# Kernel tuning notes

Measured on AMD Instinct MI355X. Metric: run time of the kernel, lower is better.

## Reference

```python
import jax, jax.numpy as jnp
import numpy as np

N = 100000
E = 1600000
D_IN = 128
D_H = 128
D_OUT = 128
LN_EPS = 1e-5
NORM_EPS = 1e-12


def _sage_conv(x, src, dst, Wl, bl, Wr):
    # PyG SAGEConv(mean): out = lin_l(mean_{j in N(i)} x_j) + lin_r(x_i)
    msgs = x[src]                                             # [E, d] gather
    summed = jax.ops.segment_sum(msgs, dst, num_segments=N)   # [N, d]
    cnt = jax.ops.segment_sum(jnp.ones((src.shape[0],), x.dtype), dst, num_segments=N)
    mean = summed / jnp.maximum(cnt, 1.0)[:, None]
    return mean @ Wl + bl + x @ Wr


def _layer_norm(x, g, b):
    mu = jnp.mean(x, axis=-1, keepdims=True)
    var = jnp.mean(jnp.square(x - mu), axis=-1, keepdims=True)
    return (x - mu) * jax.lax.rsqrt(var + LN_EPS) * g + b


def setup_inputs() -> dict:
    key = jax.random.key(0)
    ks = jax.random.split(key, 20)
    x = jax.random.normal(ks[0], (N, D_IN), dtype=jnp.float32)
    edge_index = jax.random.randint(ks[1], (2, E), 0, N, dtype=jnp.int64)
    dims = [(D_IN, D_H), (D_H, D_H), (D_H, D_OUT)]
    inp = {"x": x, "edge_index": edge_index}
    for i, (di, do) in enumerate(dims):
        s = 1.0 / np.sqrt(di)
        inp[f"Wl{i}"] = jax.random.normal(ks[2 + 5 * i], (di, do), dtype=jnp.float32) * s
        inp[f"bl{i}"] = jnp.zeros((do,), dtype=jnp.float32)
        inp[f"Wr{i}"] = jax.random.normal(ks[3 + 5 * i], (di, do), dtype=jnp.float32) * s
        inp[f"g{i}"] = jnp.ones((do,), dtype=jnp.float32)
        inp[f"b{i}"] = jnp.zeros((do,), dtype=jnp.float32)
    return inp


def reference(x, edge_index, Wl0, bl0, Wr0, g0, b0, Wl1, bl1, Wr1, g1, b1, Wl2, bl2, Wr2, g2, b2):
    src, dst = edge_index[0], edge_index[1]
    params = [(Wl0, bl0, Wr0, g0, b0), (Wl1, bl1, Wr1, g1, b1), (Wl2, bl2, Wr2, g2, b2)]
    h = x
    for i, (Wl, bl, Wr, g, b) in enumerate(params):
        h = _sage_conv(h, src, dst, Wl, bl, Wr)
        h = _layer_norm(h, g, b)
        if i < len(params) - 1:
            h = jax.nn.elu(h)
            # dropout is identity in eval mode
    # F.normalize(p=2, dim=-1)
    nrm = jnp.sqrt(jnp.sum(jnp.square(h), axis=-1, keepdims=True))
    return h / jnp.maximum(nrm, NORM_EPS)
```

## Files before the change

### kernel.cpp

```cpp
#include <hip/hip_runtime.h>
#include <hip/hip_bf16.h>
#include <math.h>

#define N_NODES 100000
#define N_EDGES 1600000
#define D 128
#define NB 391
#define BSTRIDE 6000

#define OFF_SSRC 0
#define OFF_OFFS 6400000
#define OFF_PACK 6800016
#define OFF_GC   7193232
#define OFF_BB   7195296
#define OFF_M    7204112
#define OFF_XHI  58404112
#define OFF_XLO  84004112

#define LSTRIDE 130

typedef __attribute__((ext_vector_type(8))) short short8;
typedef __attribute__((ext_vector_type(4))) float floatx4;

__device__ __forceinline__ unsigned short f2bf(float f) {
    unsigned int u = __float_as_uint(f);
    u += 0x7fffu + ((u >> 16) & 1u);
    return (unsigned short)(u >> 16);
}
__device__ __forceinline__ float bf2f(unsigned short h) {
    return __uint_as_float(((unsigned int)h) << 16);
}

__global__ __launch_bounds__(256) void part_kernel(const int* __restrict__ src,
                                                   const int* __restrict__ dst,
                                                   int* __restrict__ gcur,
                                                   uint2* __restrict__ staging) {
    __shared__ int hist[NB];
    __shared__ int base[NB];
    int t = threadIdx.x;
    int e0 = blockIdx.x * 4096;
    for (int i = t; i < NB; i += 256) hist[i] = 0;
    __syncthreads();
    int d[16];
#pragma unroll
    for (int i = 0; i < 16; ++i) {
        int e = e0 + i * 256 + t;
        d[i] = (e < N_EDGES) ? dst[e] : -1;
        if (d[i] >= 0) atomicAdd(&hist[d[i] >> 8], 1);
    }
    __syncthreads();
    for (int i = t; i < NB; i += 256) {
        int h = hist[i];
        base[i] = h ? atomicAdd(&gcur[i], h) : 0;
    }
    __syncthreads();
    for (int i = t; i < NB; i += 256) hist[i] = 0;
    __syncthreads();
#pragma unroll
    for (int i = 0; i < 16; ++i) {
        if (d[i] >= 0) {
            int e = e0 + i * 256 + t;
            int b = d[i] >> 8;
            int slot = atomicAdd(&hist[b], 1);
            staging[b * BSTRIDE + base[b] + slot] =
                make_uint2((unsigned)src[e], (unsigned)(d[i] & 255));
        }
    }
}

__global__ void bscan_kernel(const int* __restrict__ gcur, int* __restrict__ bbase,
                             int* __restrict__ offs) {
    __shared__ int sh[512];
    int t = threadIdx.x;
    int v = (t < NB) ? gcur[t] : 0;
    sh[t] = v;
    __syncthreads();
    for (int off = 1; off < 512; off <<= 1) {
        int y = (t >= off) ? sh[t - off] : 0;
        __syncthreads();
        sh[t] += y;
        __syncthreads();
    }
    if (t < NB) bbase[t] = sh[t] - v;
    if (t == 0) offs[N_NODES] = N_EDGES;
}

__global__ __launch_bounds__(256) void bsort_kernel(const uint2* __restrict__ staging,
                                                    const int* __restrict__ gcur,
                                                    const int* __restrict__ bbase,
                                                    int* __restrict__ offs,
                                                    int* __restrict__ s_src) {
    __shared__ int cnt[256];
    __shared__ int scn[256];
    __shared__ int ssrc[BSTRIDE];
    int b = blockIdx.x;
    int t = threadIdx.x;
    int n = gcur[b];
    int base_out = bbase[b];
    cnt[t] = 0;
    __syncthreads();
    for (int e = t; e < n; e += 256) {
        uint2 v = staging[b * BSTRIDE + e];
        atomicAdd(&cnt[v.y], 1);
    }
    __syncthreads();
    int v = cnt[t];
    scn[t] = v;
    __syncthreads();
    for (int off = 1; off < 256; off <<= 1) {
        int y = (t >= off) ? scn[t - off] : 0;
        __syncthreads();
        scn[t] += y;
        __syncthreads();
    }
    int ex = scn[t] - v;
    int node = b * 256 + t;
    if (node < N_NODES) offs[node] = base_out + ex;
    cnt[t] = ex;
    __syncthreads();
    for (int e = t; e < n; e += 256) {
        uint2 w = staging[b * BSTRIDE + e];
        int slot = atomicAdd(&cnt[w.y], 1);
        ssrc[slot] = (int)w.x;
    }
    __syncthreads();
    for (int e = t; e < n; e += 256) s_src[base_out + e] = ssrc[e];
}

__global__ void pack_kernel(const float* __restrict__ Wl0, const float* __restrict__ Wr0,
                            const float* __restrict__ Wl1, const float* __restrict__ Wr1,
                            const float* __restrict__ Wl2, const float* __restrict__ Wr2,
                            unsigned short* __restrict__ pack) {
    int tid = blockIdx.x * blockDim.x + threadIdx.x;
    int l = tid >> 15;
    int r = tid & 32767;
    int k = r >> 7;
    int n = r & 127;
    const float* Wl = (l == 0) ? Wl0 : (l == 1) ? Wl1 : Wl2;
    const float* Wr = (l == 0) ? Wr0 : (l == 1) ? Wr1 : Wr2;
    float v = (k < 128) ? Wl[k * 128 + n] : Wr[(k - 128) * 128 + n];
    unsigned short hi = f2bf(v);
    unsigned short lo = f2bf(v - bf2f(hi));
    int ct = n >> 4, ks = k >> 5, lane = ((k >> 3) & 3) * 16 + (n & 15), j = k & 7;
    int idx = ((ct * 8 + ks) * 64 + lane) * 8 + j;
    pack[l * 65536 + idx] = hi;
    pack[l * 65536 + 32768 + idx] = lo;
}

__global__ __launch_bounds__(256) void cvt_kernel(const float* __restrict__ x,
                                                  unsigned int* __restrict__ Xhi,
                                                  unsigned int* __restrict__ Xlo) {
    int i = blockIdx.x * 256 + threadIdx.x;
    float2 v = ((const float2*)x)[i];
    unsigned short h0 = f2bf(v.x), h1 = f2bf(v.y);
    unsigned short l0 = f2bf(v.x - bf2f(h0)), l1 = f2bf(v.y - bf2f(h1));
    Xhi[i] = (unsigned int)h0 | ((unsigned int)h1 << 16);
    Xlo[i] = (unsigned int)l0 | ((unsigned int)l1 << 16);
}

__global__ __launch_bounds__(128) void fused_kernel(const uint4* __restrict__ X4,
                                                    const unsigned short* __restrict__ Xh,
                                                    const unsigned short* __restrict__ Xl,
                                                    unsigned short* __restrict__ XhO,
                                                    unsigned short* __restrict__ XlO,
                                                    const int* __restrict__ s_src,
                                                    const int* __restrict__ offs,
                                                    const unsigned short* __restrict__ packh,
                                                    const unsigned short* __restrict__ packl,
                                                    const float* __restrict__ bl,
                                                    const float* __restrict__ g,
                                                    const float* __restrict__ b,
                                                    float* __restrict__ outf, int last) {
    __shared__ float lmean[64 * LSTRIDE];
    int t = threadIdx.x;
    int wid = t >> 6, lane = t & 63;
    int sub = lane >> 4, li = lane & 15;
    int nodebase = blockIdx.x * 64;

    int off_l = offs[min(nodebase + wid * 32 + min(lane, 32), N_NODES)];

#define ACC_U4(u)                                                                  \
    do {                                                                           \
        const unsigned int w_[4] = {(u).x, (u).y, (u).z, (u).w};                   \
        _Pragma("unroll") for (int j_ = 0; j_ < 4; ++j_) {                         \
            acc[2 * j_]     += bf2f((unsigned short)w_[j_]);                       \
            acc[2 * j_ + 1] += bf2f((unsigned short)(w_[j_] >> 16));               \
        }                                                                          \
    } while (0)

    for (int i = 0; i < 32; ++i) {
        int lrow = wid * 32 + i;
        int beg = __shfl(off_l, i);
        int end = __shfl(off_l, i + 1);
        int deg = end - beg;
        float acc[8];
#pragma unroll
        for (int j = 0; j < 8; ++j) acc[j] = 0.f;

        for (int cbase = 0; cbase < deg; cbase += 64) {
            int cnt = min(deg - cbase, 64);
            int myidx = s_src[min(beg + cbase + lane, N_EDGES - 1)];
            int j = 0;
            for (; j + 16 <= cnt; j += 16) {
                int i0 = __shfl(myidx, j + sub);
                int i1 = __shfl(myidx, j + 4 + sub);
                int i2 = __shfl(myidx, j + 8 + sub);
                int i3 = __shfl(myidx, j + 12 + sub);
                uint4 u0 = X4[i0 * 16 + li];
                uint4 u1 = X4[i1 * 16 + li];
                uint4 u2 = X4[i2 * 16 + li];
                uint4 u3 = X4[i3 * 16 + li];
                ACC_U4(u0); ACC_U4(u1); ACC_U4(u2); ACC_U4(u3);
            }
            if (j + 8 <= cnt) {
                int i0 = __shfl(myidx, j + sub);
                int i1 = __shfl(myidx, j + 4 + sub);
                uint4 u0 = X4[i0 * 16 + li];
                uint4 u1 = X4[i1 * 16 + li];
                ACC_U4(u0); ACC_U4(u1);
                j += 8;
            }
            if (j + 4 <= cnt) {
                int i0 = __shfl(myidx, j + sub);
                uint4 u0 = X4[i0 * 16 + li];
                ACC_U4(u0);
                j += 4;
            }
            int rem = cnt - j;
            if (rem > 0) {
                int i0 = __shfl(myidx, j + min(sub, rem - 1));
                uint4 u0 = X4[i0 * 16 + li];
                if (sub < rem) ACC_U4(u0);
            }
        }
#pragma unroll
        for (int j = 0; j < 8; ++j) {
            acc[j] += __shfl_xor(acc[j], 16);
            acc[j] += __shfl_xor(acc[j], 32);
        }
        float inv = 1.0f / fmaxf((float)deg, 1.0f);
        if (sub < 2) {
            floatx4 v = {acc[sub * 4] * inv, acc[sub * 4 + 1] * inv,
                         acc[sub * 4 + 2] * inv, acc[sub * 4 + 3] * inv};
            *(floatx4*)&lmean[lrow * LSTRIDE + li * 8 + sub * 4] = v;
        }
    }
#undef ACC_U4
    __syncthreads();

    int colb = lane & 15;
    int quad = lane >> 4;
    int kq = quad * 8;
    int tilebase = nodebase + wid * 32;

    int rowA[2], lrowA[2];
    rowA[0] = min(tilebase + colb, N_NODES - 1);
    rowA[1] = min(tilebase + 16 + colb, N_NODES - 1);
    lrowA[0] = wid * 32 + colb;
    lrowA[1] = wid * 32 + 16 + colb;

    floatx4 acc[2][8];
#pragma unroll
    for (int rt = 0; rt < 2; ++rt)
#pragma unroll
        for (int ct = 0; ct < 8; ++ct) acc[rt][ct] = (floatx4){0.f, 0.f, 0.f, 0.f};

#pragma unroll
    for (int ks = 0; ks < 4; ++ks) {
        int kof = ks * 32 + kq;
        short8 ah[2], al[2];
#pragma unroll
        for (int rt = 0; rt < 2; ++rt) {
            const float* p = &lmean[lrowA[rt] * LSTRIDE + kof];
            floatx4 v0 = *(const floatx4*)p;
            floatx4 v1 = *(const floatx4*)(p + 4);
            float v[8] = {v0[0], v0[1], v0[2], v0[3], v1[0], v1[1], v1[2], v1[3]};
#pragma unroll
            for (int j = 0; j < 8; ++j) {
                unsigned short hi = f2bf(v[j]);
                ah[rt][j] = (short)hi;
                al[rt][j] = (short)f2bf(v[j] - bf2f(hi));
            }
        }
#pragma unroll
        for (int ct = 0; ct < 8; ++ct) {
            int fo = ((ct * 8 + ks) << 9) + (lane << 3);
            short8 bh = *(const short8*)(packh + fo);
            short8 bo = *(const short8*)(packl + fo);
#pragma unroll
            for (int rt = 0; rt < 2; ++rt) {
                acc[rt][ct] = __builtin_amdgcn_mfma_f32_16x16x32_bf16(ah[rt], bh, acc[rt][ct], 0, 0, 0);
                acc[rt][ct] = __builtin_amdgcn_mfma_f32_16x16x32_bf16(al[rt], bh, acc[rt][ct], 0, 0, 0);
                acc[rt][ct] = __builtin_amdgcn_mfma_f32_16x16x32_bf16(ah[rt], bo, acc[rt][ct], 0, 0, 0);
            }
        }
    }
#pragma unroll
    for (int ks = 4; ks < 8; ++ks) {
        int kof = (ks - 4) * 32 + kq;
        short8 ah[2], al[2];
#pragma unroll
        for (int rt = 0; rt < 2; ++rt) {
            long o = (long)rowA[rt] * D + kof;
            ah[rt] = *(const short8*)(Xh + o);
            al[rt] = *(const short8*)(Xl + o);
        }
#pragma unroll
        for (int ct = 0; ct < 8; ++ct) {
            int fo = ((ct * 8 + ks) << 9) + (lane << 3);
            short8 bh = *(const short8*)(packh + fo);
            short8 bo = *(const short8*)(packl + fo);
#pragma unroll
            for (int rt = 0; rt < 2; ++rt) {
                acc[rt][ct] = __builtin_amdgcn_mfma_f32_16x16x32_bf16(ah[rt], bh, acc[rt][ct], 0, 0, 0);
                acc[rt][ct] = __builtin_amdgcn_mfma_f32_16x16x32_bf16(al[rt], bh, acc[rt][ct], 0, 0, 0);
                acc[rt][ct] = __builtin_amdgcn_mfma_f32_16x16x32_bf16(ah[rt], bo, acc[rt][ct], 0, 0, 0);
            }
        }
    }

    float bb[8], gg[8], b2[8];
#pragma unroll
    for (int ct = 0; ct < 8; ++ct) {
        bb[ct] = bl[ct * 16 + colb];
        gg[ct] = g[ct * 16 + colb];
        b2[ct] = b[ct * 16 + colb];
    }

#pragma unroll
    for (int rt = 0; rt < 2; ++rt) {
#pragma unroll
        for (int ct = 0; ct < 8; ++ct)
#pragma unroll
            for (int e = 0; e < 4; ++e) acc[rt][ct][e] += bb[ct];
        float mu[4], rstd[4];
#pragma unroll
        for (int e = 0; e < 4; ++e) {
            float s = 0.f;
#pragma unroll
            for (int ct = 0; ct < 8; ++ct) s += acc[rt][ct][e];
            s += __shfl_xor(s, 1); s += __shfl_xor(s, 2);
            s += __shfl_xor(s, 4); s += __shfl_xor(s, 8);
            mu[e] = s * (1.0f / 128.0f);
        }
#pragma unroll
        for (int e = 0; e < 4; ++e) {
            float q = 0.f;
#pragma unroll
            for (int ct = 0; ct < 8; ++ct) {
                float d = acc[rt][ct][e] - mu[e];
                q += d * d;
            }
            q += __shfl_xor(q, 1); q += __shfl_xor(q, 2);
            q += __shfl_xor(q, 4); q += __shfl_xor(q, 8);
            rstd[e] = rsqrtf(q * (1.0f / 128.0f) + 1e-5f);
        }
#pragma unroll
        for (int ct = 0; ct < 8; ++ct)
#pragma unroll
            for (int e = 0; e < 4; ++e) {
                float y = (acc[rt][ct][e] - mu[e]) * rstd[e] * gg[ct] + b2[ct];
                if (!last) y = (y > 0.f) ? y : expm1f(y);
                acc[rt][ct][e] = y;
            }
        if (last) {
#pragma unroll
            for (int e = 0; e < 4; ++e) {
                float ss = 0.f;
#pragma unroll
                for (int ct = 0; ct < 8; ++ct) {
                    float y = acc[rt][ct][e];
                    ss += y * y;
                }
                ss += __shfl_xor(ss, 1); ss += __shfl_xor(ss, 2);
                ss += __shfl_xor(ss, 4); ss += __shfl_xor(ss, 8);
                float inv = 1.0f / fmaxf(sqrtf(ss), 1e-12f);
#pragma unroll
                for (int ct = 0; ct < 8; ++ct) acc[rt][ct][e] *= inv;
            }
#pragma unroll
            for (int e = 0; e < 4; ++e) {
                int row = tilebase + rt * 16 + quad * 4 + e;
                if (row < N_NODES) {
#pragma unroll
                    for (int ct = 0; ct < 8; ++ct)
                        outf[(long)row * D + ct * 16 + colb] = acc[rt][ct][e];
                }
            }
        } else {
#pragma unroll
            for (int e = 0; e < 4; ++e) {
                int row = tilebase + rt * 16 + quad * 4 + e;
                if (row < N_NODES) {
#pragma unroll
                    for (int ct = 0; ct < 8; ++ct) {
                        float y = acc[rt][ct][e];
                        unsigned short hh = f2bf(y);
                        unsigned short ll = f2bf(y - bf2f(hh));
                        long o = (long)row * D + ct * 16 + colb;
                        XhO[o] = hh;
                        XlO[o] = ll;
                    }
                }
            }
        }
    }
}

extern "C" void kernel_launch(void* const* d_in, const int* in_sizes, int n_in,
                              void* d_out, int out_size, void* d_ws, size_t ws_size,
                              hipStream_t stream) {
    const float* x = (const float*)d_in[0];
    const int* edges = (const int*)d_in[1];
    const int* src = edges;
    const int* dst = edges + N_EDGES;
    const float* Wl[3] = {(const float*)d_in[2], (const float*)d_in[7],  (const float*)d_in[12]};
    const float* bl[3] = {(const float*)d_in[3], (const float*)d_in[8],  (const float*)d_in[13]};
    const float* Wr[3] = {(const float*)d_in[4], (const float*)d_in[9],  (const float*)d_in[14]};
    const float* g[3]  = {(const float*)d_in[5], (const float*)d_in[10], (const float*)d_in[15]};
    const float* b[3]  = {(const float*)d_in[6], (const float*)d_in[11], (const float*)d_in[16]};

    char* ws = (char*)d_ws;
    int* s_src = (int*)(ws + OFF_SSRC);
    int* offs  = (int*)(ws + OFF_OFFS);
    unsigned short* wpack = (unsigned short*)(ws + OFF_PACK);
    int* gcur  = (int*)(ws + OFF_GC);
    int* bbase = (int*)(ws + OFF_BB);
    uint2* staging = (uint2*)(ws + OFF_M);
    unsigned short* XhB = (unsigned short*)(ws + OFF_M);
    unsigned short* XlB = (unsigned short*)(ws + OFF_M + 25600000);
    unsigned short* XhA = (unsigned short*)(ws + OFF_XHI);
    unsigned short* XlA = (unsigned short*)(ws + OFF_XLO);
    float* out = (float*)d_out;

    hipMemsetAsync(gcur, 0, NB * sizeof(int), stream);
    part_kernel<<<(N_EDGES + 4095) / 4096, 256, 0, stream>>>(src, dst, gcur, staging);
    bscan_kernel<<<1, 512, 0, stream>>>(gcur, bbase, offs);
    bsort_kernel<<<NB, 256, 0, stream>>>(staging, gcur, bbase, offs, s_src);
    pack_kernel<<<(3 * 32768) / 256, 256, 0, stream>>>(Wl[0], Wr[0], Wl[1], Wr[1], Wl[2], Wr[2], wpack);
    cvt_kernel<<<(N_NODES * 64) / 256, 256, 0, stream>>>(x, (unsigned int*)XhA, (unsigned int*)XlA);

    const int FB = (N_NODES + 63) / 64;
    unsigned short* ph[3] = {wpack, wpack + 65536, wpack + 131072};

    fused_kernel<<<FB, 128, 0, stream>>>((const uint4*)XhA, XhA, XlA, XhB, XlB,
                                         s_src, offs, ph[0], ph[0] + 32768,
                                         bl[0], g[0], b[0], nullptr, 0);
    fused_kernel<<<FB, 128, 0, stream>>>((const uint4*)XhB, XhB, XlB, XhA, XlA,
                                         s_src, offs, ph[1], ph[1] + 32768,
                                         bl[1], g[1], b[1], nullptr, 0);
    fused_kernel<<<FB, 128, 0, stream>>>((const uint4*)XhA, XhA, XlA, nullptr, nullptr,
                                         s_src, offs, ph[2], ph[2] + 32768,
                                         bl[2], g[2], b[2], out, 1);
}
```

Baseline: 720.0 us.

## Split fused SAGE kernel into 4 waves of 16 rows, swizzle LDS, drop barrier

Each block now runs 4 waves, each owning 16 node rows for both the neighbor-mean gather and the MFMA projection, instead of 2 waves with 32 rows each. Because each wave reads only the LDS rows it wrote, the block barrier is removed, and LDS padding is replaced with an XOR swizzle. The goal is more concurrent waves to hide gather latency and higher occupancy via launch bounds. The cost is that weight fragments are reloaded per 16-row tile, doubling weight traffic per row.

```diff
diff --git a/kernel.cpp b/kernel.cpp
--- a/kernel.cpp
+++ b/kernel.cpp
@@ -16,8 +16,6 @@
 #define OFF_M    7204112
 #define OFF_XHI  58404112
 #define OFF_XLO  84004112
-
-#define LSTRIDE 130
 
 typedef __attribute__((ext_vector_type(8))) short short8;
 typedef __attribute__((ext_vector_type(4))) float floatx4;
@@ -158,26 +156,26 @@
     Xlo[i] = (unsigned int)l0 | ((unsigned int)l1 << 16);
 }
 
-__global__ __launch_bounds__(128) void fused_kernel(const uint4* __restrict__ X4,
-                                                    const unsigned short* __restrict__ Xh,
-                                                    const unsigned short* __restrict__ Xl,
-                                                    unsigned short* __restrict__ XhO,
-                                                    unsigned short* __restrict__ XlO,
-                                                    const int* __restrict__ s_src,
-                                                    const int* __restrict__ offs,
-                                                    const unsigned short* __restrict__ packh,
-                                                    const unsigned short* __restrict__ packl,
-                                                    const float* __restrict__ bl,
-                                                    const float* __restrict__ g,
-                                                    const float* __restrict__ b,
-                                                    float* __restrict__ outf, int last) {
-    __shared__ float lmean[64 * LSTRIDE];
+__global__ __launch_bounds__(256, 5) void fused_kernel(const uint4* __restrict__ X4,
+                                                       const unsigned short* __restrict__ Xh,
+                                                       const unsigned short* __restrict__ Xl,
+                                                       unsigned short* __restrict__ XhO,
+                                                       unsigned short* __restrict__ XlO,
+                                                       const int* __restrict__ s_src,
+                                                       const int* __restrict__ offs,
+                                                       const unsigned short* __restrict__ packh,
+                                                       const unsigned short* __restrict__ packl,
+                                                       const float* __restrict__ bl,
+                                                       const float* __restrict__ g,
+                                                       const float* __restrict__ b,
+                                                       float* __restrict__ outf, int last) {
+    __shared__ float lmean[64 * 128];
     int t = threadIdx.x;
     int wid = t >> 6, lane = t & 63;
     int sub = lane >> 4, li = lane & 15;
     int nodebase = blockIdx.x * 64;
 
-    int off_l = offs[min(nodebase + wid * 32 + min(lane, 32), N_NODES)];
+    int off_l = offs[min(nodebase + wid * 16 + min(lane, 16), N_NODES)];
 
 #define ACC_U4(u)                                                                  \
     do {                                                                           \
@@ -188,8 +186,8 @@
         }                                                                          \
     } while (0)
 
-    for (int i = 0; i < 32; ++i) {
-        int lrow = wid * 32 + i;
+    for (int i = 0; i < 16; ++i) {
+        int lrow = wid * 16 + i;
         int beg = __shfl(off_l, i);
         int end = __shfl(off_l, i + 1);
         int deg = end - beg;
@@ -240,46 +238,40 @@
         }
         float inv = 1.0f / fmaxf((float)deg, 1.0f);
         if (sub < 2) {
+            int chunk = li * 2 + sub;
             floatx4 v = {acc[sub * 4] * inv, acc[sub * 4 + 1] * inv,
                          acc[sub * 4 + 2] * inv, acc[sub * 4 + 3] * inv};
-            *(floatx4*)&lmean[lrow * LSTRIDE + li * 8 + sub * 4] = v;
+            *(floatx4*)&lmean[lrow * 128 + ((chunk ^ (lrow & 7)) << 2)] = v;
         }
     }
 #undef ACC_U4
-    __syncthreads();
 
     int colb = lane & 15;
     int quad = lane >> 4;
     int kq = quad * 8;
-    int tilebase = nodebase + wid * 32;
-
-    int rowA[2], lrowA[2];
-    rowA[0] = min(tilebase + colb, N_NODES - 1);
-    rowA[1] = min(tilebase + 16 + colb, N_NODES - 1);
-    lrowA[0] = wid * 32 + colb;
-    lrowA[1] = wid * 32 + 16 + colb;
-
-    floatx4 acc[2][8];
-#pragma unroll
-    for (int rt = 0; rt < 2; ++rt)
-#pragma unroll
-        for (int ct = 0; ct < 8; ++ct) acc[rt][ct] = (floatx4){0.f, 0.f, 0.f, 0.f};
+    int tilebase = nodebase + wid * 16;
+
+    int rowA = min(tilebase + colb, N_NODES - 1);
+    int lrowA = wid * 16 + colb;
+    int rsalt = lrowA & 7;
+
+    floatx4 acc[8];
+#pragma unroll
+    for (int ct = 0; ct < 8; ++ct) acc[ct] = (floatx4){0.f, 0.f, 0.f, 0.f};
 
 #pragma unroll
     for (int ks = 0; ks < 4; ++ks) {
-        int kof = ks * 32 + kq;
-        short8 ah[2], al[2];
-#pragma unroll
-        for (int rt = 0; rt < 2; ++rt) {
-            const float* p = &lmean[lrowA[rt] * LSTRIDE + kof];
-            floatx4 v0 = *(const floatx4*)p;
-            floatx4 v1 = *(const floatx4*)(p + 4);
+        int chunk0 = ks * 8 + quad * 2;
+        short8 ah, al;
+        {
+            floatx4 v0 = *(const floatx4*)&lmean[lrowA * 128 + ((chunk0 ^ rsalt) << 2)];
+            floatx4 v1 = *(const floatx4*)&lmean[lrowA * 128 + (((chunk0 + 1) ^ rsalt) << 2)];
             float v[8] = {v0[0], v0[1], v0[2], v0[3], v1[0], v1[1], v1[2], v1[3]};
 #pragma unroll
             for (int j = 0; j < 8; ++j) {
                 unsigned short hi = f2bf(v[j]);
-                ah[rt][j] = (short)hi;
-                al[rt][j] = (short)f2bf(v[j] - bf2f(hi));
+                ah[j] = (short)hi;
+                al[j] = (short)f2bf(v[j] - bf2f(hi));
             }
         }
 #pragma unroll
@@ -287,35 +279,25 @@
             int fo = ((ct * 8 + ks) << 9) + (lane << 3);
             short8 bh = *(const short8*)(packh + fo);
             short8 bo = *(const short8*)(packl + fo);
-#pragma unroll
-            for (int rt = 0; rt < 2; ++rt) {
-                acc[rt][ct] = __builtin_amdgcn_mfma_f32_16x16x32_bf16(ah[rt], bh, acc[rt][ct], 0, 0, 0);
-                acc[rt][ct] = __builtin_amdgcn_mfma_f32_16x16x32_bf16(al[rt], bh, acc[rt][ct], 0, 0, 0);
-                acc[rt][ct] = __builtin_amdgcn_mfma_f32_16x16x32_bf16(ah[rt], bo, acc[rt][ct], 0, 0, 0);
-            }
+            acc[ct] = __builtin_amdgcn_mfma_f32_16x16x32_bf16(ah, bh, acc[ct], 0, 0, 0);
+            acc[ct] = __builtin_amdgcn_mfma_f32_16x16x32_bf16(al, bh, acc[ct], 0, 0, 0);
+            acc[ct] = __builtin_amdgcn_mfma_f32_16x16x32_bf16(ah, bo, acc[ct], 0, 0, 0);
         }
     }
 #pragma unroll
     for (int ks = 4; ks < 8; ++ks) {
         int kof = (ks - 4) * 32 + kq;
-        short8 ah[2], al[2];
-#pragma unroll
-        for (int rt = 0; rt < 2; ++rt) {
-            long o = (long)rowA[rt] * D + kof;
-            ah[rt] = *(const short8*)(Xh + o);
-            al[rt] = *(const short8*)(Xl + o);
-        }
+        long o = (long)rowA * D + kof;
+        short8 ah = *(const short8*)(Xh + o);
+        short8 al = *(const short8*)(Xl + o);
 #pragma unroll
         for (int ct = 0; ct < 8; ++ct) {
             int fo = ((ct * 8 + ks) << 9) + (lane << 3);
             short8 bh = *(const short8*)(packh + fo);
             short8 bo = *(const short8*)(packl + fo);
-#pragma unroll
-            for (int rt = 0; rt < 2; ++rt) {
-                acc[rt][ct] = __builtin_amdgcn_mfma_f32_16x16x32_bf16(ah[rt], bh, acc[rt][ct], 0, 0, 0);
-                acc[rt][ct] = __builtin_amdgcn_mfma_f32_16x16x32_bf16(al[rt], bh, acc[rt][ct], 0, 0, 0);
-                acc[rt][ct] = __builtin_amdgcn_mfma_f32_16x16x32_bf16(ah[rt], bo, acc[rt][ct], 0, 0, 0);
-            }
+            acc[ct] = __builtin_amdgcn_mfma_f32_16x16x32_bf16(ah, bh, acc[ct], 0, 0, 0);
+            acc[ct] = __builtin_amdgcn_mfma_f32_16x16x32_bf16(al, bh, acc[ct], 0, 0, 0);
+            acc[ct] = __builtin_amdgcn_mfma_f32_16x16x32_bf16(ah, bo, acc[ct], 0, 0, 0);
         }
     }
 
@@ -328,79 +310,76 @@
     }
 
 #pragma unroll
-    for (int rt = 0; rt < 2; ++rt) {
-#pragma unroll
-        for (int ct = 0; ct < 8; ++ct)
-#pragma unroll
-            for (int e = 0; e < 4; ++e) acc[rt][ct][e] += bb[ct];
-        float mu[4], rstd[4];
+    for (int ct = 0; ct < 8; ++ct)
+#pragma unroll
+        for (int e = 0; e < 4; ++e) acc[ct][e] += bb[ct];
+    float mu[4], rstd[4];
+#pragma unroll
+    for (int e = 0; e < 4; ++e) {
+        float s = 0.f;
+#pragma unroll
+        for (int ct = 0; ct < 8; ++ct) s += acc[ct][e];
+        s += __shfl_xor(s, 1); s += __shfl_xor(s, 2);
+        s += __shfl_xor(s, 4); s += __shfl_xor(s, 8);
+        mu[e] = s * (1.0f / 128.0f);
+    }
+#pragma unroll
+    for (int e = 0; e < 4; ++e) {
+        float q = 0.f;
+#pragma unroll
+        for (int ct = 0; ct < 8; ++ct) {
+            float d = acc[ct][e] - mu[e];
+            q += d * d;
+        }
+        q += __shfl_xor(q, 1); q += __shfl_xor(q, 2);
+        q += __shfl_xor(q, 4); q += __shfl_xor(q, 8);
+        rstd[e] = rsqrtf(q * (1.0f / 128.0f) + 1e-5f);
+    }
+#pragma unroll
+    for (int ct = 0; ct < 8; ++ct)
 #pragma unroll
         for (int e = 0; e < 4; ++e) {
-            float s = 0.f;
-#pragma unroll
-            for (int ct = 0; ct < 8; ++ct) s += acc[rt][ct][e];
-            s += __shfl_xor(s, 1); s += __shfl_xor(s, 2);
-            s += __shfl_xor(s, 4); s += __shfl_xor(s, 8);
-            mu[e] = s * (1.0f / 128.0f);
-        }
+            float y = (acc[ct][e] - mu[e]) * rstd[e] * gg[ct] + b2[ct];
+            if (!last) y = (y > 0.f) ? y : expm1f(y);
+            acc[ct][e] = y;
+        }
+    if (last) {
 #pragma unroll
         for (int e = 0; e < 4; ++e) {
-            float q = 0.f;
+            float ss = 0.f;
 #pragma unroll
             for (int ct = 0; ct < 8; ++ct) {
-                float d = acc[rt][ct][e] - mu[e];
-                q += d * d;
-            }
-            q += __shfl_xor(q, 1); q += __shfl_xor(q, 2);
-            q += __shfl_xor(q, 4); q += __shfl_xor(q, 8);
-            rstd[e] = rsqrtf(q * (1.0f / 128.0f) + 1e-5f);
-        }
-#pragma unroll
-        for (int ct = 0; ct < 8; ++ct)
-#pragma unroll
-            for (int e = 0; e < 4; ++e) {
-                float y = (acc[rt][ct][e] - mu[e]) * rstd[e] * gg[ct] + b2[ct];
-                if (!last) y = (y > 0.f) ? y : expm1f(y);
-                acc[rt][ct][e] = y;
-            }
-        if (last) {
-#pragma unroll
-            for (int e = 0; e < 4; ++e) {
-                float ss = 0.f;
+                float y = acc[ct][e];
+                ss += y * y;
+            }
+            ss += __shfl_xor(ss, 1); ss += __shfl_xor(ss, 2);
+            ss += __shfl_xor(ss, 4); ss += __shfl_xor(ss, 8);
+            float inv = 1.0f / fmaxf(sqrtf(ss), 1e-12f);
+#pragma unroll
+            for (int ct = 0; ct < 8; ++ct) acc[ct][e] *= inv;
+        }
+#pragma unroll
+        for (int e = 0; e < 4; ++e) {
+            int row = tilebase + quad * 4 + e;
+            if (row < N_NODES) {
+#pragma unroll
+                for (int ct = 0; ct < 8; ++ct)
+                    outf[(long)row * D + ct * 16 + colb] = acc[ct][e];
+            }
+        }
+    } else {
+#pragma unroll
+        for (int e = 0; e < 4; ++e) {
+            int row = tilebase + quad * 4 + e;
+            if (row < N_NODES) {
 #pragma unroll
                 for (int ct = 0; ct < 8; ++ct) {
-                    float y = acc[rt][ct][e];
-                    ss += y * y;
-                }
-                ss += __shfl_xor(ss, 1); ss += __shfl_xor(ss, 2);
-                ss += __shfl_xor(ss, 4); ss += __shfl_xor(ss, 8);
-                float inv = 1.0f / fmaxf(sqrtf(ss), 1e-12f);
-#pragma unroll
-                for (int ct = 0; ct < 8; ++ct) acc[rt][ct][e] *= inv;
-            }
-#pragma unroll
-            for (int e = 0; e < 4; ++e) {
-                int row = tilebase + rt * 16 + quad * 4 + e;
-                if (row < N_NODES) {
-#pragma unroll
-                    for (int ct = 0; ct < 8; ++ct)
-                        outf[(long)row * D + ct * 16 + colb] = acc[rt][ct][e];
-                }
-            }
-        } else {
-#pragma unroll
-            for (int e = 0; e < 4; ++e) {
-                int row = tilebase + rt * 16 + quad * 4 + e;
-                if (row < N_NODES) {
-#pragma unroll
-                    for (int ct = 0; ct < 8; ++ct) {
-                        float y = acc[rt][ct][e];
-                        unsigned short hh = f2bf(y);
-                        unsigned short ll = f2bf(y - bf2f(hh));
-                        long o = (long)row * D + ct * 16 + colb;
-                        XhO[o] = hh;
-                        XlO[o] = ll;
-                    }
+                    float y = acc[ct][e];
+                    unsigned short hh = f2bf(y);
+                    unsigned short ll = f2bf(y - bf2f(hh));
+                    long o = (long)row * D + ct * 16 + colb;
+                    XhO[o] = hh;
+                    XlO[o] = ll;
                 }
             }
         }
@@ -443,13 +422,13 @@
     const int FB = (N_NODES + 63) / 64;
     unsigned short* ph[3] = {wpack, wpack + 65536, wpack + 131072};
 
-    fused_kernel<<<FB, 128, 0, stream>>>((const uint4*)XhA, XhA, XlA, XhB, XlB,
+    fused_kernel<<<FB, 256, 0, stream>>>((const uint4*)XhA, XhA, XlA, XhB, XlB,
                                          s_src, offs, ph[0], ph[0] + 32768,
                                          bl[0], g[0], b[0], nullptr, 0);
-    fused_kernel<<<FB, 128, 0, stream>>>((const uint4*)XhB, XhB, XlB, XhA, XlA,
+    fused_kernel<<<FB, 256, 0, stream>>>((const uint4*)XhB, XhB, XlB, XhA, XlA,
                                          s_src, offs, ph[1], ph[1] + 32768,
                                          bl[1], g[1], b[1], nullptr, 0);
-    fused_kernel<<<FB, 128, 0, stream>>>((const uint4*)XhA, XhA, XlA, nullptr, nullptr,
+    fused_kernel<<<FB, 256, 0, stream>>>((const uint4*)XhA, XhA, XlA, nullptr, nullptr,
                                          s_src, offs, ph[2], ph[2] + 32768,
                                          bl[2], g[2], b[2], out, 1);
 }
```

After: 592.0 us. 17.8% less time.
